# Kernel tuning notes

Hardware: AMD Instinct MI355X
Metric: run time of the kernel (lower is better)

Reference implementation:

```python
import jax, jax.numpy as jnp
import numpy as np

B, S, NH, D_IN = 64, 512, 4, 256   # batch, seq_len, rnn n_head, input_dim
H = 256                            # hidden_dim == attention activation_dim
AH = 256                           # attention_hidden_dim (attn out_dim)
OUT = 3                            # output_dim (sentiment classes)


def setup_inputs() -> dict:
    key = jax.random.key(0)
    ks = jax.random.split(key, 9)
    def p(k, shape, scale=0.05):
        return jax.random.normal(k, shape, dtype=jnp.float32) * scale
    return dict(
        x=jax.random.normal(ks[0], (B, S, NH, D_IN), dtype=jnp.float32),
        Wk=p(ks[1], (D_IN, H)), bk=jnp.zeros((H,), jnp.float32),
        Wq=p(ks[2], (H, H)),    bq=jnp.zeros((H,), jnp.float32),
        w_mlp=p(ks[3], (2 * H,)),
        Wproj=p(ks[4], (H, AH)), bproj=jnp.zeros((AH,), jnp.float32),
        W1=p(ks[5], (D_IN + AH, H)), b1=jnp.zeros((H,), jnp.float32),
        W2=p(ks[6], (H, H)),    b2=jnp.zeros((H,), jnp.float32),
        Wo=p(ks[7], (NH * H, OUT)), bo=jnp.zeros((OUT,), jnp.float32),
    )


def _cell(x_t, hidden, params):
    Wk, bk, Wq, bq, w_mlp, Wproj, bproj, W1, b1, W2, b2, Wo, bo = params
    kx = x_t @ Wk + bk           # [B, NH, H]  keys from step input
    qx = hidden @ Wq + bq        # [B, NH, H]  queries from hidden state
    w1, w2 = w_mlp[:H], w_mlp[H:]
    # MLP score: s[b,i,j] = tanh(cat(kx[b,j], qx[b,i]) . w) = tanh(kx[b,j].w1 + qx[b,i].w2)
    score = jnp.tanh((qx @ w2)[:, :, None] + (kx @ w1)[:, None, :])  # [B, NH, NH]
    score = jax.nn.softmax(score, axis=-1)
    attn = jnp.einsum('bij,bjh->bih', score, kx) @ Wproj + bproj     # [B, NH, AH]
    concat = jnp.concatenate([x_t, attn], axis=-1)                   # [B, NH, D_IN+AH]
    hidden_new = jax.nn.relu(concat @ W1 + b1) @ W2 + b2             # [B, NH, H]
    logits = hidden_new.reshape(B, NH * H) @ Wo + bo                 # [B, OUT]
    out = jax.nn.log_softmax(logits, axis=-1)
    return out, hidden_new


def reference(x, Wk, bk, Wq, bq, w_mlp, Wproj, bproj, W1, b1, W2, b2, Wo, bo):
    params = (Wk, bk, Wq, bq, w_mlp, Wproj, bproj, W1, b1, W2, b2, Wo, bo)
    h0 = jnp.zeros((B, NH, H), x.dtype)
    xs = jnp.swapaxes(x, 0, 1)  # [S, B, NH, D_IN] for scan over time
    def step(h, x_t):
        out, h_new = _cell(x_t, h, params)
        return h_new, out
    h_final, outs = jax.lax.scan(step, h0, xs)
    # return_sequence=False: last-step log-softmax output and final hidden
    return outs[-1], h_final
```

## Files before the change

### kernel.cpp

```cpp
#include <hip/hip_runtime.h>
#include <hip/hip_bf16.h>
#include <math.h>

#define BB   64
#define SS   512
#define NHH  4
#define DD   256
#define HH   256
#define LDH  264

typedef __attribute__((ext_vector_type(8))) short  short8;
typedef __attribute__((ext_vector_type(4))) float  floatx4;


__device__ __forceinline__ unsigned short f2b(float f) {
  __hip_bfloat16 h = __float2bfloat16(f);
  return __builtin_bit_cast(unsigned short, h);
}
__device__ __forceinline__ float b2f(unsigned short u) {
  unsigned v = (unsigned)u << 16;
  return __builtin_bit_cast(float, v);
}

__global__ __launch_bounds__(256) void init1_kernel(
    const float* __restrict__ Wk, const float* __restrict__ Wproj,
    const float* __restrict__ W1, const float* __restrict__ Wq,
    const float* __restrict__ bq, const float* __restrict__ w_mlp,
    const float* __restrict__ W2, const float* __restrict__ b2,
    const float* __restrict__ bk,
    float* __restrict__ ws, unsigned short* __restrict__ wpack)
{
  __shared__ float vsh[256];
  __shared__ float red[256];
  int tid = threadIdx.x;
  int b = blockIdx.x;

  if (b == 0) {
    const float* w2 = w_mlp + HH;
    {
      float a = 0.f;
      const float4* Wq4 = (const float4*)(Wq + tid * 256);
      const float4* w24 = (const float4*)w2;
      for (int k = 0; k < 64; ++k) {
        float4 wv = Wq4[k], xv = w24[k];
        a = fmaf(wv.x, xv.x, fmaf(wv.y, xv.y, fmaf(wv.z, xv.z, fmaf(wv.w, xv.w, a))));
      }
      vsh[tid] = a;
    }
    __syncthreads();
    {
      float a2 = 0.f;
      const float4* W24 = (const float4*)(W2 + tid * 256);
      const float4* v4  = (const float4*)vsh;
      for (int k = 0; k < 64; ++k) {
        float4 wv = W24[k], xv = v4[k];
        a2 = fmaf(wv.x, xv.x, fmaf(wv.y, xv.y, fmaf(wv.z, xv.z, fmaf(wv.w, xv.w, a2))));
      }
      ws[tid] = 2.f * a2;
    }
    red[tid] = bq[tid] * w_mlp[HH + tid];
    __syncthreads();
    for (int s = 128; s; s >>= 1) { if (tid < s) red[tid] += red[tid + s]; __syncthreads(); }
    float c = red[0];
    __syncthreads();
    ws[768 + tid] = 2.f * c;
    red[tid] = b2[tid] * vsh[tid];
    __syncthreads();
    for (int s = 128; s; s >>= 1) { if (tid < s) red[tid] += red[tid + s]; __syncthreads(); }
    if (tid == 0) ws[512] = 2.f * (red[0] + c);
    __syncthreads();
    red[tid] = bk[tid] * w_mlp[tid];
    __syncthreads();
    for (int s = 128; s; s >>= 1) { if (tid < s) red[tid] += red[tid + s]; __syncthreads(); }
    if (tid == 0) ws[513] = 2.f * red[0];
    return;
  }

  if (b <= 256) {
    int idx = (b - 1) * 256 + tid;
    int j    = idx & 7;
    int lane = (idx >> 3) & 63;
    int ks   = (idx >> 9) & 7;
    int pan  = idx >> 12;
    int k = ks * 32 + ((lane >> 4) << 3) + j;
    int n = pan * 16 + (lane & 15);
    wpack[idx] = f2b(W1[k * 256 + n]);
    return;
  }

  {
    int r = b - 257;
    const float* w1b = W1 + 256 * 256;
    float acc = 0.f;
    for (int k = 0; k < 256; ++k)
      acc = fmaf(Wproj[r * 256 + k], w1b[k * 256 + tid], acc);
    ws[132096 + r * 256 + tid] = acc;
  }
}

__global__ __launch_bounds__(256) void init2_kernel(
    const float* __restrict__ Wk, const float* __restrict__ W1,
    const float* __restrict__ bproj, const float* __restrict__ bk,
    const float* __restrict__ w_mlp, const float* __restrict__ b1,
    float* __restrict__ ws, unsigned short* __restrict__ wpack)
{
  __shared__ float red[256];
  int tid = threadIdx.x;
  int b = blockIdx.x;
  const float* Wc = ws + 132096;

  if (b < 256) {
    int r = b;
    float acc = 0.f;
    for (int k = 0; k < 256; ++k)
      acc = fmaf(Wk[r * 256 + k], Wc[k * 256 + tid], acc);
    int n = tid;
    int pan = n >> 4, ks = r >> 5, j = r & 7;
    int lane = ((r >> 3) & 3) * 16 + (n & 15);
    wpack[65536 + pan * 4096 + ks * 512 + lane * 8 + j] = f2b(acc);
    red[tid] = Wk[r * 256 + tid] * w_mlp[tid];
    __syncthreads();
    for (int s = 128; s; s >>= 1) { if (tid < s) red[tid] += red[tid + s]; __syncthreads(); }
    if (tid == 0) ws[197632 + r] = 2.f * red[0];
    return;
  }

  {
    const float* w1b = W1 + 256 * 256;
    float a3 = 0.f;
    for (int k = 0; k < 256; ++k)
      a3 = fmaf(bproj[k], w1b[k * 256 + tid], a3);
    for (int k = 0; k < 256; ++k)
      a3 = fmaf(bk[k], Wc[k * 256 + tid], a3);
    ws[256 + tid] = a3;
    ws[197888 + tid] = a3 + b1[tid];
  }
}

__device__ __forceinline__ void mfma_gemm4(
    const unsigned short* A_lds, const short8* __restrict__ Bp,
    const float* __restrict__ bias, floatx4 acc[4][4], int l, int w)
{
  int col = l & 15, quad = l >> 4;
#pragma unroll
  for (int pp = 0; pp < 4; ++pp) {
    float bv = bias ? bias[(w * 4 + pp) * 16 + col] : 0.f;
#pragma unroll
    for (int mf = 0; mf < 4; ++mf)
      acc[mf][pp] = (floatx4){bv, bv, bv, bv};
  }
  const short8* Bb = Bp + (size_t)(w * 4) * 512 + l;
  short8 bb[3][4];
  short8 aa[2][4];
#pragma unroll
  for (int pp = 0; pp < 4; ++pp) bb[0][pp] = Bb[pp * 512];
#pragma unroll
  for (int pp = 0; pp < 4; ++pp) bb[1][pp] = Bb[pp * 512 + 64];
#pragma unroll
  for (int mf = 0; mf < 4; ++mf)
    aa[0][mf] = *(const short8*)(A_lds + (mf * 16 + col) * LDH + quad * 8);
#pragma unroll
  for (int kb = 0; kb < 8; ++kb) {
    if (kb + 2 < 8) {
#pragma unroll
      for (int pp = 0; pp < 4; ++pp)
        bb[(kb + 2) % 3][pp] = Bb[pp * 512 + (kb + 2) * 64];
    }
    if (kb + 1 < 8) {
#pragma unroll
      for (int mf = 0; mf < 4; ++mf)
        aa[(kb + 1) & 1][mf] =
            *(const short8*)(A_lds + (mf * 16 + col) * LDH + (kb + 1) * 32 + quad * 8);
    }
#pragma unroll
    for (int mf = 0; mf < 4; ++mf)
#pragma unroll
      for (int pp = 0; pp < 4; ++pp)
        acc[mf][pp] = __builtin_amdgcn_mfma_f32_16x16x32_bf16(
            aa[kb & 1][mf], bb[kb % 3][pp], acc[mf][pp], 0, 0, 0);
  }
}

__device__ __forceinline__ void acc_to_global_bf16(
    unsigned short* __restrict__ dst, const floatx4 acc[4][4],
    int l, int w, int b, int tt)
{
  int col = l & 15, quad = l >> 4;
#pragma unroll
  for (int mf = 0; mf < 4; ++mf)
#pragma unroll
    for (int r = 0; r < 4; ++r) {
      int m2 = mf * 16 + quad * 4 + r;
      size_t base = (((size_t)(tt * 16 + (m2 >> 2)) * 64 + b) * 4 + (m2 & 3)) * 256;
#pragma unroll
      for (int pp = 0; pp < 4; ++pp)
        dst[base + (w * 4 + pp) * 16 + col] = f2b(acc[mf][pp][r]);
    }
}

__device__ void precompute_block(
    int px, const float* __restrict__ x, const unsigned short* __restrict__ wpack,
    const float* __restrict__ ws,
    float* __restrict__ kw_c, unsigned short* __restrict__ xw1_c,
    unsigned short* __restrict__ kpw_c, int t0, char* smem)
{
  float* kwbuf = (float*)smem;
  unsigned short* XS = (unsigned short*)(smem + 2048);

  int b  = px & 63;
  int tt = px >> 6;
  int tid = threadIdx.x;
  int l = tid & 63, w = tid >> 6;

  const float4* xsrc = (const float4*)(x + (size_t)(b * SS + t0 + tt * 16) * NHH * DD);
#pragma unroll
  for (int i = 0; i < 16; ++i) {
    int f4 = i * 256 + tid;
    int r = f4 >> 6, c4 = f4 & 63;
    float4 v = xsrc[f4];
    ushort4 h;
    h.x = f2b(v.x); h.y = f2b(v.y); h.z = f2b(v.z); h.w = f2b(v.w);
    *(ushort4*)&XS[r * LDH + c4 * 4] = h;
  }
  __syncthreads();

  const short8* wpA = (const short8*)(wpack);
  const short8* wpD = (const short8*)(wpack + 65536);

  {
    const float* wkw = ws + 197632;
    float part = 0.f;
    const unsigned short* trow = XS + l * LDH + w * 64;
#pragma unroll
    for (int j8 = 0; j8 < 8; ++j8) {
      short8 tv = *(const short8*)(trow + j8 * 8);
#pragma unroll
      for (int j = 0; j < 8; ++j)
        part = fmaf(b2f((unsigned short)tv[j]), wkw[w * 64 + j8 * 8 + j], part);
    }
    kwbuf[l * 4 + w] = part;
  }

  floatx4 acc[4][4];

  mfma_gemm4(XS, wpA, ws + 197888, acc, l, w);
  acc_to_global_bf16(xw1_c, acc, l, w, b, tt);

  mfma_gemm4(XS, wpD, nullptr, acc, l, w);
  acc_to_global_bf16(kpw_c, acc, l, w, b, tt);

  __syncthreads();
  if (tid < 64) {
    float s = kwbuf[tid * 4] + kwbuf[tid * 4 + 1] + kwbuf[tid * 4 + 2] + kwbuf[tid * 4 + 3]
            + ws[513];
    kw_c[((size_t)(tt * 16 + (tid >> 2)) * 64 + b) * 4 + (tid & 3)] = s;
  }
}

__device__ __forceinline__ float wave_reduce_sum(float x) {
#define DPPSTEP(ctrl, rmask)                                                   \
  {                                                                            \
    int _s = __builtin_amdgcn_update_dpp(0, __builtin_bit_cast(int, x),        \
                                         (ctrl), (rmask), 0xf, true);          \
    x += __builtin_bit_cast(float, _s);                                        \
  }
  DPPSTEP(0x111, 0xf)
  DPPSTEP(0x112, 0xf)
  DPPSTEP(0x114, 0xf)
  DPPSTEP(0x118, 0xf)
  DPPSTEP(0x142, 0xa)
  DPPSTEP(0x143, 0xc)
#undef DPPSTEP
  return __builtin_bit_cast(float, __builtin_amdgcn_readlane(__builtin_bit_cast(int, x), 63));
}

__device__ void seq_block(
    const unsigned short* __restrict__ xw1_c, const unsigned short* __restrict__ kpw_c,
    const float* __restrict__ kw_c, float* __restrict__ ws,
    float* __restrict__ relu_u, int t0, int n)
{
  int b = blockIdx.x;
  int tid = threadIdx.x;
  int i = tid >> 6, l = tid & 63;

  float4 v2v = ((const float4*)ws)[l];
  float c2s = ws[512];
  float qw2 = ws[768 + b * 4 + i];

  struct Slot { ushort4 x, k0, k1, k2, k3; float4 kw; };
  struct SP { const ushort4 *xp, *kp; const float4 *kw; };

  const ushort4* xw4 = (const ushort4*)xw1_c;
  const ushort4* kp4 = (const ushort4*)kpw_c;
  const float4*  kw4 = (const float4*)kw_c;

  SP p0 = { xw4 + (b * 4 + i) * 64 + l, kp4 + b * 256 + l, kw4 + b };
  SP p1 = { p0.xp + 16384, p0.kp + 16384, p0.kw + 64 };
  SP p2 = { p1.xp + 16384, p1.kp + 16384, p1.kw + 64 };
  SP p3 = { p2.xp + 16384, p2.kp + 16384, p2.kw + 64 };

  auto refill = [&](Slot& s, SP& p) {
    s.x  = *p.xp;
    s.k0 = p.kp[0];
    s.k1 = p.kp[64];
    s.k2 = p.kp[128];
    s.k3 = p.kp[192];
    s.kw = *p.kw;
    p.xp += 65536; p.kp += 65536; p.kw += 256;
  };

  auto step = [&](Slot& s, int t) {
    float r0 = __builtin_amdgcn_rcpf(__expf(qw2 + s.kw.x) + 1.f);
    float r1 = __builtin_amdgcn_rcpf(__expf(qw2 + s.kw.y) + 1.f);
    float r2 = __builtin_amdgcn_rcpf(__expf(qw2 + s.kw.z) + 1.f);
    float r3 = __builtin_amdgcn_rcpf(__expf(qw2 + s.kw.w) + 1.f);
    float q0 = __expf(fmaf(-2.f, r0, 1.f));
    float q1 = __expf(fmaf(-2.f, r1, 1.f));
    float q2 = __expf(fmaf(-2.f, r2, 1.f));
    float q3 = __expf(fmaf(-2.f, r3, 1.f));
    float inv = __builtin_amdgcn_rcpf((q0 + q1) + (q2 + q3));
    float4 K0 = {b2f(s.k0.x), b2f(s.k0.y), b2f(s.k0.z), b2f(s.k0.w)};
    float4 K1 = {b2f(s.k1.x), b2f(s.k1.y), b2f(s.k1.z), b2f(s.k1.w)};
    float4 K2 = {b2f(s.k2.x), b2f(s.k2.y), b2f(s.k2.z), b2f(s.k2.w)};
    float4 K3 = {b2f(s.k3.x), b2f(s.k3.y), b2f(s.k3.z), b2f(s.k3.w)};
    float4 X  = {b2f(s.x.x), b2f(s.x.y), b2f(s.x.z), b2f(s.x.w)};
    float4 a;
    a.x = fmaf(q0, K0.x, fmaf(q1, K1.x, fmaf(q2, K2.x, q3 * K3.x)));
    a.y = fmaf(q0, K0.y, fmaf(q1, K1.y, fmaf(q2, K2.y, q3 * K3.y)));
    a.z = fmaf(q0, K0.z, fmaf(q1, K1.z, fmaf(q2, K2.z, q3 * K3.z)));
    a.w = fmaf(q0, K0.w, fmaf(q1, K1.w, fmaf(q2, K2.w, q3 * K3.w)));
    float4 u;
    u.x = fmaf(a.x, inv, X.x); u.y = fmaf(a.y, inv, X.y);
    u.z = fmaf(a.z, inv, X.z); u.w = fmaf(a.w, inv, X.w);
    float4 rr;
    rr.x = fmaxf(u.x, 0.f); rr.y = fmaxf(u.y, 0.f);
    rr.z = fmaxf(u.z, 0.f); rr.w = fmaxf(u.w, 0.f);
    float d = fmaf(rr.x, v2v.x, rr.y * v2v.y) + fmaf(rr.z, v2v.z, rr.w * v2v.w);
    qw2 = wave_reduce_sum(d) + c2s;
    if (t0 + t == SS - 1)
      *(float4*)&relu_u[(size_t)(b * 4 + i) * 256 + l * 4] = rr;
  };

  Slot s0, s1, s2, s3;
  refill(s0, p0); refill(s1, p1); refill(s2, p2); refill(s3, p3);
  for (int t = 0; t < n; t += 4) {
    step(s0, t);     refill(s0, p0);
    step(s1, t + 1); refill(s1, p1);
    step(s2, t + 2); refill(s2, p2);
    step(s3, t + 3); refill(s3, p3);
  }
  if (l == 0) ws[768 + b * 4 + i] = qw2;
}

__global__ __launch_bounds__(256, 1) void fused_kernel(
    const float* __restrict__ x, const unsigned short* __restrict__ wpack,
    float* kwB, unsigned short* xw1B, unsigned short* kpwB, int t0_pre,
    const float* kwA, const unsigned short* xw1A, const unsigned short* kpwA,
    int t0_seq, int n_seq,
    float* __restrict__ ws, float* __restrict__ relu_u)
{
  __shared__ __align__(16) char smem[2048 + 64 * LDH * 2];
  if (blockIdx.x < 64) {
    if (n_seq > 0) seq_block(xw1A, kpwA, kwA, ws, relu_u, t0_seq, n_seq);
    return;
  }
  precompute_block(blockIdx.x - 64, x, wpack, ws,
                   kwB, xw1B, kpwB, t0_pre, smem);
}

__global__ __launch_bounds__(256) void final_hidden_kernel(
    const float* __restrict__ relu_u, const float* __restrict__ W2,
    const float* __restrict__ b2, float* __restrict__ out)
{
  __shared__ float rs[256];
  int row = blockIdx.x;
  int tid = threadIdx.x;
  rs[tid] = relu_u[(size_t)row * 256 + tid];
  __syncthreads();
  float acc = b2[tid];
  for (int k = 0; k < 256; ++k) acc = fmaf(rs[k], W2[k * 256 + tid], acc);
  out[192 + (size_t)row * 256 + tid] = acc;
}

__global__ __launch_bounds__(256) void final_logits_kernel(
    const float* __restrict__ hf, const float* __restrict__ Wo,
    const float* __restrict__ bo, float* __restrict__ outp)
{
  __shared__ float r0[256], r1[256], r2[256];
  int b = blockIdx.x;
  int tid = threadIdx.x;
  float a0 = 0.f, a1 = 0.f, a2 = 0.f;
  for (int k = tid; k < 1024; k += 256) {
    float h = hf[(size_t)b * 1024 + k];
    a0 = fmaf(h, Wo[k * 3 + 0], a0);
    a1 = fmaf(h, Wo[k * 3 + 1], a1);
    a2 = fmaf(h, Wo[k * 3 + 2], a2);
  }
  r0[tid] = a0; r1[tid] = a1; r2[tid] = a2;
  __syncthreads();
  for (int s = 128; s; s >>= 1) {
    if (tid < s) { r0[tid] += r0[tid + s]; r1[tid] += r1[tid + s]; r2[tid] += r2[tid + s]; }
    __syncthreads();
  }
  if (tid == 0) {
    float l0 = r0[0] + bo[0], l1 = r1[0] + bo[1], l2 = r2[0] + bo[2];
    float m = fmaxf(l0, fmaxf(l1, l2));
    float lse = m + logf(expf(l0 - m) + expf(l1 - m) + expf(l2 - m));
    outp[b * 3 + 0] = l0 - lse;
    outp[b * 3 + 1] = l1 - lse;
    outp[b * 3 + 2] = l2 - lse;
  }
}

extern "C" void kernel_launch(void* const* d_in, const int* in_sizes, int n_in,
                              void* d_out, int out_size, void* d_ws, size_t ws_size,
                              hipStream_t stream)
{
  const float* x     = (const float*)d_in[0];
  const float* Wk    = (const float*)d_in[1];
  const float* bk    = (const float*)d_in[2];
  const float* Wq    = (const float*)d_in[3];
  const float* bq    = (const float*)d_in[4];
  const float* w_mlp = (const float*)d_in[5];
  const float* Wproj = (const float*)d_in[6];
  const float* bproj = (const float*)d_in[7];
  const float* W1    = (const float*)d_in[8];
  const float* b1    = (const float*)d_in[9];
  const float* W2    = (const float*)d_in[10];
  const float* b2    = (const float*)d_in[11];
  const float* Wo    = (const float*)d_in[12];
  const float* bo    = (const float*)d_in[13];
  float* out = (float*)d_out;
  float* ws  = (float*)d_ws;

  float* ru = ws + 1024;
  unsigned short* wpack = (unsigned short*)(ws + 66560);
  const size_t OFF_CH = 198144;
  const long per_t = 256 + 2 * 32768;

  long ws_floats = (long)(ws_size / 4);
  long avail = ws_floats - (long)OFF_CH - 8L * per_t;

  int Tc = 128;
  while (Tc > 0 && 2L * Tc * per_t > avail) Tc -= 16;
  bool pipelined = (Tc >= 16);
  if (!pipelined) {
    Tc = 128;
    while (Tc > 16 && (long)Tc * per_t > avail) Tc -= 16;
  }

  float* bufA = ws + OFF_CH;
  float* bufB = pipelined ? bufA + (size_t)Tc * per_t : bufA;

  auto kw_of  = [&](float* base) { return base; };
  auto xw_of  = [&](float* base) { return (unsigned short*)(base + (size_t)Tc * 256); };
  auto kpw_of = [&](float* base) {
    return (unsigned short*)(base + (size_t)Tc * 256) + (size_t)Tc * 65536;
  };

  init1_kernel<<<513, 256, 0, stream>>>(Wk, Wproj, W1, Wq, bq, w_mlp, W2, b2, bk,
                                        ws, wpack);
  init2_kernel<<<257, 256, 0, stream>>>(Wk, W1, bproj, bk, w_mlp, b1, ws, wpack);

  int C = (SS + Tc - 1) / Tc;

  if (pipelined) {
    for (int r = 0; r <= C; ++r) {
      bool hasPre = (r < C);
      bool hasSeq = (r >= 1);
      int t0p = r * Tc;
      int np  = hasPre ? ((SS - t0p) < Tc ? (SS - t0p) : Tc) : 0;
      int t0s = (r - 1) * Tc;
      int ns  = hasSeq ? ((SS - t0s) < Tc ? (SS - t0s) : Tc) : 0;
      float* pB = ((r & 1) ? bufB : bufA);
      float* pA = (((r - 1) & 1) ? bufB : bufA);
      int grid = 64 + (hasPre ? 64 * (np / 16) : 0);
      fused_kernel<<<grid, 256, 0, stream>>>(
          x, wpack,
          kw_of(pB), xw_of(pB), kpw_of(pB), t0p,
          kw_of(pA), xw_of(pA), kpw_of(pA), t0s, ns,
          ws, ru);
    }
  } else {
    for (int c = 0; c < C; ++c) {
      int t0 = c * Tc;
      int n = (SS - t0) < Tc ? (SS - t0) : Tc;
      fused_kernel<<<64 + 64 * (n / 16), 256, 0, stream>>>(
          x, wpack,
          kw_of(bufA), xw_of(bufA), kpw_of(bufA), t0,
          kw_of(bufA), xw_of(bufA), kpw_of(bufA), 0, 0,
          ws, ru);
      fused_kernel<<<64, 256, 0, stream>>>(
          x, wpack,
          kw_of(bufA), xw_of(bufA), kpw_of(bufA), t0,
          kw_of(bufA), xw_of(bufA), kpw_of(bufA), t0, n,
          ws, ru);
    }
  }

  final_hidden_kernel<<<BB * NHH, 256, 0, stream>>>(ru, W2, b2, out);
  final_logits_kernel<<<BB, 256, 0, stream>>>(out + 192, Wo, bo, out);
}
```

Measured before the change: 415.5 us.

## Replace chunked pipelined launches with single precompute and one-wave-per-row sequential kernel

Drops the chunked double-buffered scheme, where each launch fused precompute blocks for the next time chunk with sequential blocks for the current one. The new code precomputes all 512 timesteps in one large kernel, then runs the recurrence in a single kernel of 256 one-wave blocks, one per (batch, head) row. This removes multiple launches and the per-chunk carry of qw2 state, and spreads the serial scan over more CUs. The cost is losing overlap between precompute and the recurrence, and needing a much larger workspace for the full precomputed buffers, with no fallback if the workspace is smaller.

Result: slower. 499.9 us (+20.3%).

```diff
diff --git a/kernel.cpp b/kernel.cpp
--- a/kernel.cpp
+++ b/kernel.cpp
@@ -12,6 +12,9 @@
 typedef __attribute__((ext_vector_type(8))) short  short8;
 typedef __attribute__((ext_vector_type(4))) float  floatx4;
 
+#define OFF_KW   198144
+#define OFF_XW   (OFF_KW + 131072)
+#define OFF_KPW  (OFF_XW + 8388608)
 
 __device__ __forceinline__ unsigned short f2b(float f) {
   __hip_bfloat16 h = __float2bfloat16(f);
@@ -198,21 +201,25 @@
     }
 }
 
-__device__ void precompute_block(
-    int px, const float* __restrict__ x, const unsigned short* __restrict__ wpack,
-    const float* __restrict__ ws,
-    float* __restrict__ kw_c, unsigned short* __restrict__ xw1_c,
-    unsigned short* __restrict__ kpw_c, int t0, char* smem)
-{
+__global__ __launch_bounds__(256, 1) void precompute_kernel(
+    const float* __restrict__ x, const unsigned short* __restrict__ wpack,
+    float* __restrict__ ws)
+{
+  __shared__ __align__(16) char smem[2048 + 64 * LDH * 2];
   float* kwbuf = (float*)smem;
   unsigned short* XS = (unsigned short*)(smem + 2048);
 
+  int px = blockIdx.x;
   int b  = px & 63;
   int tt = px >> 6;
   int tid = threadIdx.x;
   int l = tid & 63, w = tid >> 6;
 
-  const float4* xsrc = (const float4*)(x + (size_t)(b * SS + t0 + tt * 16) * NHH * DD);
+  float* kw_c = ws + OFF_KW;
+  unsigned short* xw1_c = (unsigned short*)(ws + OFF_XW);
+  unsigned short* kpw_c = (unsigned short*)(ws + OFF_KPW);
+
+  const float4* xsrc = (const float4*)(x + (size_t)(b * SS + tt * 16) * NHH * DD);
 #pragma unroll
   for (int i = 0; i < 16; ++i) {
     int f4 = i * 256 + tid;
@@ -274,14 +281,14 @@
   return __builtin_bit_cast(float, __builtin_amdgcn_readlane(__builtin_bit_cast(int, x), 63));
 }
 
-__device__ void seq_block(
+__global__ __launch_bounds__(64) void seq_kernel(
     const unsigned short* __restrict__ xw1_c, const unsigned short* __restrict__ kpw_c,
     const float* __restrict__ kw_c, float* __restrict__ ws,
-    float* __restrict__ relu_u, int t0, int n)
-{
-  int b = blockIdx.x;
-  int tid = threadIdx.x;
-  int i = tid >> 6, l = tid & 63;
+    float* __restrict__ relu_u)
+{
+  int c = blockIdx.x;
+  int b = c >> 2, i = c & 3;
+  int l = threadIdx.x;
 
   float4 v2v = ((const float4*)ws)[l];
   float c2s = ws[512];
@@ -337,35 +344,18 @@
     rr.z = fmaxf(u.z, 0.f); rr.w = fmaxf(u.w, 0.f);
     float d = fmaf(rr.x, v2v.x, rr.y * v2v.y) + fmaf(rr.z, v2v.z, rr.w * v2v.w);
     qw2 = wave_reduce_sum(d) + c2s;
-    if (t0 + t == SS - 1)
+    if (t == SS - 1)
       *(float4*)&relu_u[(size_t)(b * 4 + i) * 256 + l * 4] = rr;
   };
 
   Slot s0, s1, s2, s3;
   refill(s0, p0); refill(s1, p1); refill(s2, p2); refill(s3, p3);
-  for (int t = 0; t < n; t += 4) {
+  for (int t = 0; t < SS; t += 4) {
     step(s0, t);     refill(s0, p0);
     step(s1, t + 1); refill(s1, p1);
     step(s2, t + 2); refill(s2, p2);
     step(s3, t + 3); refill(s3, p3);
   }
-  if (l == 0) ws[768 + b * 4 + i] = qw2;
-}
-
-__global__ __launch_bounds__(256, 1) void fused_kernel(
-    const float* __restrict__ x, const unsigned short* __restrict__ wpack,
-    float* kwB, unsigned short* xw1B, unsigned short* kpwB, int t0_pre,
-    const float* kwA, const unsigned short* xw1A, const unsigned short* kpwA,
-    int t0_seq, int n_seq,
-    float* __restrict__ ws, float* __restrict__ relu_u)
-{
-  __shared__ __align__(16) char smem[2048 + 64 * LDH * 2];
-  if (blockIdx.x < 64) {
-    if (n_seq > 0) seq_block(xw1A, kpwA, kwA, ws, relu_u, t0_seq, n_seq);
-    return;
-  }
-  precompute_block(blockIdx.x - 64, x, wpack, ws,
-                   kwB, xw1B, kpwB, t0_pre, smem);
 }
 
 __global__ __launch_bounds__(256) void final_hidden_kernel(
@@ -435,68 +425,17 @@
 
   float* ru = ws + 1024;
   unsigned short* wpack = (unsigned short*)(ws + 66560);
-  const size_t OFF_CH = 198144;
-  const long per_t = 256 + 2 * 32768;
-
-  long ws_floats = (long)(ws_size / 4);
-  long avail = ws_floats - (long)OFF_CH - 8L * per_t;
-
-  int Tc = 128;
-  while (Tc > 0 && 2L * Tc * per_t > avail) Tc -= 16;
-  bool pipelined = (Tc >= 16);
-  if (!pipelined) {
-    Tc = 128;
-    while (Tc > 16 && (long)Tc * per_t > avail) Tc -= 16;
-  }
-
-  float* bufA = ws + OFF_CH;
-  float* bufB = pipelined ? bufA + (size_t)Tc * per_t : bufA;
-
-  auto kw_of  = [&](float* base) { return base; };
-  auto xw_of  = [&](float* base) { return (unsigned short*)(base + (size_t)Tc * 256); };
-  auto kpw_of = [&](float* base) {
-    return (unsigned short*)(base + (size_t)Tc * 256) + (size_t)Tc * 65536;
-  };
+
+  float* kw_c = ws + OFF_KW;
+  unsigned short* xw1_c = (unsigned short*)(ws + OFF_XW);
+  unsigned short* kpw_c = (unsigned short*)(ws + OFF_KPW);
 
   init1_kernel<<<513, 256, 0, stream>>>(Wk, Wproj, W1, Wq, bq, w_mlp, W2, b2, bk,
                                         ws, wpack);
   init2_kernel<<<257, 256, 0, stream>>>(Wk, W1, bproj, bk, w_mlp, b1, ws, wpack);
 
-  int C = (SS + Tc - 1) / Tc;
-
-  if (pipelined) {
-    for (int r = 0; r <= C; ++r) {
-      bool hasPre = (r < C);
-      bool hasSeq = (r >= 1);
-      int t0p = r * Tc;
-      int np  = hasPre ? ((SS - t0p) < Tc ? (SS - t0p) : Tc) : 0;
-      int t0s = (r - 1) * Tc;
-      int ns  = hasSeq ? ((SS - t0s) < Tc ? (SS - t0s) : Tc) : 0;
-      float* pB = ((r & 1) ? bufB : bufA);
-      float* pA = (((r - 1) & 1) ? bufB : bufA);
-      int grid = 64 + (hasPre ? 64 * (np / 16) : 0);
-      fused_kernel<<<grid, 256, 0, stream>>>(
-          x, wpack,
-          kw_of(pB), xw_of(pB), kpw_of(pB), t0p,
-          kw_of(pA), xw_of(pA), kpw_of(pA), t0s, ns,
-          ws, ru);
-    }
-  } else {
-    for (int c = 0; c < C; ++c) {
-      int t0 = c * Tc;
-      int n = (SS - t0) < Tc ? (SS - t0) : Tc;
-      fused_kernel<<<64 + 64 * (n / 16), 256, 0, stream>>>(
-          x, wpack,
-          kw_of(bufA), xw_of(bufA), kpw_of(bufA), t0,
-          kw_of(bufA), xw_of(bufA), kpw_of(bufA), 0, 0,
-          ws, ru);
-      fused_kernel<<<64, 256, 0, stream>>>(
-          x, wpack,
-          kw_of(bufA), xw_of(bufA), kpw_of(bufA), t0,
-          kw_of(bufA), xw_of(bufA), kpw_of(bufA), t0, n,
-          ws, ru);
-    }
-  }
+  precompute_kernel<<<2048, 256, 0, stream>>>(x, wpack, ws);
+  seq_kernel<<<256, 64, 0, stream>>>(xw1_c, kpw_c, kw_c, ws, ru);
 
   final_hidden_kernel<<<BB * NHH, 256, 0, stream>>>(ru, W2, b2, out);
   final_logits_kernel<<<BB, 256, 0, stream>>>(out + 192, Wo, bo, out);
```
